# Kernel optimization log

Measured on AMD Instinct MI355X. Metric: run time of the kernel, lower is better.

## Reference

```python
import jax, jax.numpy as jnp
import numpy as np

T, B, IN_DIM, D_VALUE, D_KEY = 1024, 8, 512, 64, 64
EPS = 1e-8

def setup_inputs() -> dict:
    key = jax.random.key(0)
    ks = jax.random.split(key, 7)
    s = 1.0 / np.sqrt(IN_DIM)
    return {
        "x":  jax.random.normal(ks[0], (T, B, IN_DIM), dtype=jnp.float32),
        "Wv": jax.random.uniform(ks[1], (D_VALUE, IN_DIM), jnp.float32, -s, s),
        "bv": jax.random.uniform(ks[2], (D_VALUE,), jnp.float32, -s, s),
        "Wk": jax.random.uniform(ks[3], (D_KEY, IN_DIM), jnp.float32, -s, s),
        "bk": jax.random.uniform(ks[4], (D_KEY,), jnp.float32, -s, s),
        "Wa": jax.random.uniform(ks[5], (D_KEY, IN_DIM), jnp.float32, -s, s),
        "ba": jax.random.uniform(ks[6], (D_KEY,), jnp.float32, -s, s),
    }

def reference(x, Wv, bv, Wk, bk, Wa, ba):
    # Projections: x (T,B,in_dim) -> v (T,B,d), k (T,B,n), alpha (T,B,n)
    v = jnp.einsum('tbi,di->tbd', x, Wv) + bv
    k = jnp.einsum('tbi,ni->tbn', x, Wk) + bk
    alpha = jax.nn.sigmoid(jnp.einsum('tbi,ni->tbn', x, Wa) + ba)
    # outer product per timestep: (T,B,d,n)
    outer = jnp.einsum('tbd,tbn->tbdn', v, k)
    # log-space cumulative decay, normalized by final cumprod
    log_cumprod = jnp.cumsum(jnp.log(jnp.maximum(alpha, EPS)), axis=0)  # (T,B,n)
    cumprod = jnp.exp(log_cumprod)
    decay = cumprod / (cumprod[-1:] + EPS)
    weighted = outer * decay[:, :, None, :]  # (T,B,d,n)
    S = jnp.cumsum(weighted, axis=0)
    return S
```

## Files before the change

kernel.cpp:

```cpp
#include <hip/hip_runtime.h>
#include <math.h>

#define T_DIM  1024
#define B_DIM  8
#define IN_D   512
#define NROWS  (T_DIM * B_DIM)
#define EPSF   1e-8f
#define LOG_EPS (-18.4206807f)

#define CHUNK  16
#define NCHUNK (T_DIM / CHUNK)
#define SEG    16
#define NSEG   (T_DIM / SEG)

typedef float vfloat4 __attribute__((ext_vector_type(4)));

#define OFF_WT   0
#define OFF_V    (OFF_WT + IN_D * 192)
#define OFF_K    (OFF_V  + NROWS * 64)
#define OFF_Z    (OFF_K  + NROWS * 64)
#define OFF_SEG  (OFF_Z  + NROWS * 64)
#define OFF_TOT  (OFF_SEG + NSEG * B_DIM * 64)
#define OFF_P    (OFF_TOT + B_DIM * 64)

__global__ void k0_wt(const float* __restrict__ Wv, const float* __restrict__ Wk,
                      const float* __restrict__ Wa, float* __restrict__ Wt,
                      float* __restrict__ seg) {
    int idx = blockIdx.x * 256 + threadIdx.x;
    if (idx < NSEG * 512) seg[idx] = 0.f;
    int i = idx / 192, c = idx % 192;
    float v;
    if (c < 64)       v = Wv[c * IN_D + i];
    else if (c < 128) v = Wk[(c - 64) * IN_D + i];
    else              v = Wa[(c - 128) * IN_D + i];
    Wt[i * 192 + c] = v;
}

__global__ __launch_bounds__(256) void k1_proj(
        const float* __restrict__ x, const float* __restrict__ Wt,
        const float* __restrict__ bv, const float* __restrict__ bk, const float* __restrict__ ba,
        float* __restrict__ V, float* __restrict__ Kb, float* __restrict__ Zb,
        float* __restrict__ seg) {
    __shared__ float xs[2][32][32];
    __shared__ float wsm[2][32][192];
    const int tid  = threadIdx.x;
    const int h    = tid >> 7;
    const int t7   = tid & 127;
    const int rq   = t7 >> 4;
    const int cq   = t7 & 15;
    const int row0 = blockIdx.x * 32;

    float4 acc[4][3];
#pragma unroll
    for (int j = 0; j < 4; ++j)
#pragma unroll
        for (int m = 0; m < 3; ++m) acc[j][m] = make_float4(0.f, 0.f, 0.f, 0.f);

    for (int s = 0; s < 8; ++s) {
#pragma unroll
        for (int q = 0; q < 2; ++q) {
            int idx = tid + q * 256;
            int hh = idx >> 8, r = idx & 31, f = (idx >> 5) & 7;
            float4 v4 = reinterpret_cast<const float4*>(x)[((row0 + r) * IN_D + hh * 256 + s * 32 + f * 4) >> 2];
            xs[hh][f * 4 + 0][r] = v4.x;
            xs[hh][f * 4 + 1][r] = v4.y;
            xs[hh][f * 4 + 2][r] = v4.z;
            xs[hh][f * 4 + 3][r] = v4.w;
        }
#pragma unroll
        for (int q = 0; q < 12; ++q) {
            int idx = tid + q * 256;
            int hh = idx / 1536;
            int rem = idx - hh * 1536;
            int kk = rem / 48;
            int f  = rem - kk * 48;
            float4 v4 = reinterpret_cast<const float4*>(Wt)[((hh * 256 + s * 32 + kk) * 192 + f * 4) >> 2];
            *reinterpret_cast<float4*>(&wsm[hh][kk][f * 4]) = v4;
        }
        __syncthreads();

#pragma unroll 4
        for (int kk = 0; kk < 32; ++kk) {
            float4 xv = *reinterpret_cast<const float4*>(&xs[h][kk][rq * 4]);
#pragma unroll
            for (int m = 0; m < 3; ++m) {
                float4 wq = *reinterpret_cast<const float4*>(&wsm[h][kk][m * 64 + cq * 4]);
#pragma unroll
                for (int j = 0; j < 4; ++j) {
                    float xx = (&xv.x)[j];
                    acc[j][m].x = fmaf(xx, wq.x, acc[j][m].x);
                    acc[j][m].y = fmaf(xx, wq.y, acc[j][m].y);
                    acc[j][m].z = fmaf(xx, wq.z, acc[j][m].z);
                    acc[j][m].w = fmaf(xx, wq.w, acc[j][m].w);
                }
            }
        }
        __syncthreads();
    }

    float* red = &wsm[0][0][0];
    if (h == 1) {
#pragma unroll
        for (int j = 0; j < 4; ++j)
#pragma unroll
            for (int m = 0; m < 3; ++m)
                *reinterpret_cast<float4*>(&red[t7 * 52 + (j * 3 + m) * 4]) = acc[j][m];
    }
    __syncthreads();
    if (h == 0) {
        float4 bv4 = *reinterpret_cast<const float4*>(&bv[cq * 4]);
        float4 bk4 = *reinterpret_cast<const float4*>(&bk[cq * 4]);
        float4 ba4 = *reinterpret_cast<const float4*>(&ba[cq * 4]);
#pragma unroll
        for (int j = 0; j < 4; ++j) {
            int row = row0 + rq * 4 + j;
            float4 o0 = *reinterpret_cast<const float4*>(&red[t7 * 52 + (j * 3 + 0) * 4]);
            float4 o1 = *reinterpret_cast<const float4*>(&red[t7 * 52 + (j * 3 + 1) * 4]);
            float4 o2 = *reinterpret_cast<const float4*>(&red[t7 * 52 + (j * 3 + 2) * 4]);
            float4 r0, r1, z2, l4;
            r0.x = acc[j][0].x + o0.x + bv4.x; r0.y = acc[j][0].y + o0.y + bv4.y;
            r0.z = acc[j][0].z + o0.z + bv4.z; r0.w = acc[j][0].w + o0.w + bv4.w;
            r1.x = acc[j][1].x + o1.x + bk4.x; r1.y = acc[j][1].y + o1.y + bk4.y;
            r1.z = acc[j][1].z + o1.z + bk4.z; r1.w = acc[j][1].w + o1.w + bk4.w;
            z2.x = acc[j][2].x + o2.x + ba4.x; z2.y = acc[j][2].y + o2.y + ba4.y;
            z2.z = acc[j][2].z + o2.z + ba4.z; z2.w = acc[j][2].w + o2.w + ba4.w;
            l4.x = fmaxf(-log1pf(expf(-z2.x)), LOG_EPS);
            l4.y = fmaxf(-log1pf(expf(-z2.y)), LOG_EPS);
            l4.z = fmaxf(-log1pf(expf(-z2.z)), LOG_EPS);
            l4.w = fmaxf(-log1pf(expf(-z2.w)), LOG_EPS);
            *reinterpret_cast<float4*>(&V [row * 64 + cq * 4]) = r0;
            *reinterpret_cast<float4*>(&Kb[row * 64 + cq * 4]) = r1;
            *reinterpret_cast<float4*>(&Zb[row * 64 + cq * 4]) = l4;
            int sg = row >> 7;
            float* sp = &seg[sg * 512 + (row & 7) * 64 + cq * 4];
            atomicAdd(sp + 0, l4.x);
            atomicAdd(sp + 1, l4.y);
            atomicAdd(sp + 2, l4.z);
            atomicAdd(sp + 3, l4.w);
        }
    }
}


__global__ __launch_bounds__(256) void k3_partial(const float* __restrict__ V,
                                                  const float* __restrict__ Z,
                                                  const float* __restrict__ seg,
                                                  const float* __restrict__ Kb,
                                                  float* __restrict__ P) {
    __shared__ float vs[CHUNK * 64];
    __shared__ float wsh[CHUNK * 64];
    __shared__ float gsum[4 * 64];
    int b = blockIdx.x & 7, cch = blockIdx.x >> 3;
    int tid = threadIdx.x;
    int dg = tid >> 4, n4 = tid & 15;
    int n = tid & 63, g = tid >> 6;
    int base = b * 64 + n;

    int il = tid >> 4, f = tid & 15;
    float4 v4 = reinterpret_cast<const float4*>(V)[((cch * CHUNK + il) * 8 + b) * 16 + f];

    float run = 0.f, total = 0.f;
#pragma unroll 8
    for (int s2 = 0; s2 < NSEG; ++s2) {
        float sv = seg[s2 * 512 + base];
        if (s2 < cch) run += sv;
        total += sv;
    }
    float invden = 1.f / (expf(total) + EPSF);

    int t0 = cch * CHUNK + g * 4;
    float l0 = Z[(t0 + 0) * 512 + base];
    float l1 = Z[(t0 + 1) * 512 + base];
    float l2 = Z[(t0 + 2) * 512 + base];
    float l3 = Z[(t0 + 3) * 512 + base];
    float k0v = Kb[(t0 + 0) * 512 + base];
    float k1v = Kb[(t0 + 1) * 512 + base];
    float k2v = Kb[(t0 + 2) * 512 + base];
    float k3v = Kb[(t0 + 3) * 512 + base];
    gsum[g * 64 + n] = l0 + l1 + l2 + l3;
    reinterpret_cast<float4*>(vs)[il * 16 + f] = v4;
    __syncthreads();
    float pre = run;
#pragma unroll
    for (int g2 = 0; g2 < 3; ++g2) if (g2 < g) pre += gsum[g2 * 64 + n];
    float c0 = pre + l0, c1 = c0 + l1, c2 = c1 + l2, c3 = c2 + l3;
    wsh[(g * 4 + 0) * 64 + n] = k0v * expf(c0) * invden;
    wsh[(g * 4 + 1) * 64 + n] = k1v * expf(c1) * invden;
    wsh[(g * 4 + 2) * 64 + n] = k2v * expf(c2) * invden;
    wsh[(g * 4 + 3) * 64 + n] = k3v * expf(c3) * invden;
    __syncthreads();

    float4 acc[4];
#pragma unroll
    for (int q = 0; q < 4; ++q) acc[q] = make_float4(0.f, 0.f, 0.f, 0.f);

#pragma unroll
    for (int i = 0; i < CHUNK; ++i) {
        float4 wv = reinterpret_cast<const float4*>(wsh)[i * 16 + n4];
#pragma unroll
        for (int q = 0; q < 4; ++q) {
            float vd = vs[i * 64 + dg + 16 * q];
            acc[q].x = fmaf(vd, wv.x, acc[q].x);
            acc[q].y = fmaf(vd, wv.y, acc[q].y);
            acc[q].z = fmaf(vd, wv.z, acc[q].z);
            acc[q].w = fmaf(vd, wv.w, acc[q].w);
        }
    }
    float* Pp = P + (cch * 8 + b) * 4096;
#pragma unroll
    for (int q = 0; q < 4; ++q)
        *reinterpret_cast<float4*>(Pp + (dg + 16 * q) * 64 + 4 * n4) = acc[q];
}

__global__ __launch_bounds__(256) void k4_prefix(float* __restrict__ P) {
    int gid = blockIdx.x * 256 + threadIdx.x;
    int b = gid >> 12, dn = gid & 4095;
    float run = 0.f;
#pragma unroll
    for (int c = 0; c < NCHUNK; ++c) {
        float v = P[(c * 8 + b) * 4096 + dn];
        P[(c * 8 + b) * 4096 + dn] = run;
        run += v;
    }
}

__global__ __launch_bounds__(256) void k5_main(const float* __restrict__ V,
                                               const float* __restrict__ Z,
                                               const float* __restrict__ seg,
                                               const float* __restrict__ Kb,
                                               const float* __restrict__ P,
                                               float* __restrict__ S) {
    __shared__ float vs[CHUNK * 64];
    __shared__ float wsh[CHUNK * 64];
    __shared__ float gsum[4 * 64];
    int b = blockIdx.x & 7, cch = blockIdx.x >> 3;
    int tid = threadIdx.x;
    int dg = tid >> 4, n4 = tid & 15;
    int n = tid & 63, g = tid >> 6;
    int base = b * 64 + n;

    int il = tid >> 4, f = tid & 15;
    float4 v4 = reinterpret_cast<const float4*>(V)[((cch * CHUNK + il) * 8 + b) * 16 + f];
    vfloat4 acc[4];
    const float* Pp = P + (cch * 8 + b) * 4096;
#pragma unroll
    for (int q = 0; q < 4; ++q)
        acc[q] = *reinterpret_cast<const vfloat4*>(Pp + (dg + 16 * q) * 64 + 4 * n4);

    float run = 0.f, total = 0.f;
#pragma unroll 8
    for (int s2 = 0; s2 < NSEG; ++s2) {
        float sv = seg[s2 * 512 + base];
        if (s2 < cch) run += sv;
        total += sv;
    }
    float invden = 1.f / (expf(total) + EPSF);

    int t0 = cch * CHUNK + g * 4;
    float l0 = Z[(t0 + 0) * 512 + base];
    float l1 = Z[(t0 + 1) * 512 + base];
    float l2 = Z[(t0 + 2) * 512 + base];
    float l3 = Z[(t0 + 3) * 512 + base];
    float k0v = Kb[(t0 + 0) * 512 + base];
    float k1v = Kb[(t0 + 1) * 512 + base];
    float k2v = Kb[(t0 + 2) * 512 + base];
    float k3v = Kb[(t0 + 3) * 512 + base];
    gsum[g * 64 + n] = l0 + l1 + l2 + l3;
    reinterpret_cast<float4*>(vs)[il * 16 + f] = v4;
    __syncthreads();
    float pre = run;
#pragma unroll
    for (int g2 = 0; g2 < 3; ++g2) if (g2 < g) pre += gsum[g2 * 64 + n];
    float c0 = pre + l0, c1 = c0 + l1, c2 = c1 + l2, c3 = c2 + l3;
    wsh[(g * 4 + 0) * 64 + n] = k0v * expf(c0) * invden;
    wsh[(g * 4 + 1) * 64 + n] = k1v * expf(c1) * invden;
    wsh[(g * 4 + 2) * 64 + n] = k2v * expf(c2) * invden;
    wsh[(g * 4 + 3) * 64 + n] = k3v * expf(c3) * invden;
    __syncthreads();

#pragma unroll
    for (int i = 0; i < CHUNK; ++i) {
        float4 wv = reinterpret_cast<const float4*>(wsh)[i * 16 + n4];
        int t = cch * CHUNK + i;
        float* Sb = S + (size_t)t * 32768 + b * 4096;
#pragma unroll
        for (int q = 0; q < 4; ++q) {
            float vd = vs[i * 64 + dg + 16 * q];
            acc[q].x = fmaf(vd, wv.x, acc[q].x);
            acc[q].y = fmaf(vd, wv.y, acc[q].y);
            acc[q].z = fmaf(vd, wv.z, acc[q].z);
            acc[q].w = fmaf(vd, wv.w, acc[q].w);
            __builtin_nontemporal_store(acc[q],
                reinterpret_cast<vfloat4*>(Sb + (dg + 16 * q) * 64 + 4 * n4));
        }
    }
}

extern "C" void kernel_launch(void* const* d_in, const int* in_sizes, int n_in,
                              void* d_out, int out_size, void* d_ws, size_t ws_size,
                              hipStream_t stream) {
    const float* x  = (const float*)d_in[0];
    const float* Wv = (const float*)d_in[1];
    const float* bv = (const float*)d_in[2];
    const float* Wk = (const float*)d_in[3];
    const float* bk = (const float*)d_in[4];
    const float* Wa = (const float*)d_in[5];
    const float* ba = (const float*)d_in[6];
    float* S  = (float*)d_out;
    float* ws = (float*)d_ws;

    float* Wt  = ws + OFF_WT;
    float* V   = ws + OFF_V;
    float* Kb  = ws + OFF_K;
    float* Zb  = ws + OFF_Z;
    float* seg = ws + OFF_SEG;
    float* P   = ws + OFF_P;

    k0_wt     <<<384, 256, 0, stream>>>(Wv, Wk, Wa, Wt, seg);
    k1_proj   <<<256, 256, 0, stream>>>(x, Wt, bv, bk, ba, V, Kb, Zb, seg);
    k3_partial<<<512, 256, 0, stream>>>(V, Zb, seg, Kb, P);
    k4_prefix <<<128, 256, 0, stream>>>(P);
    k5_main   <<<512, 256, 0, stream>>>(V, Zb, seg, Kb, P, S);
}
```

Before: 216.4 us.

## Split projection K across four waves with 8-row tiles; cache decay weights for main kernel

Measured after the change: 219.6 us. About the same (+1.5%).

```diff
diff --git a/kernel.cpp b/kernel.cpp
--- a/kernel.cpp
+++ b/kernel.cpp
@@ -22,6 +22,11 @@
 #define OFF_SEG  (OFF_Z  + NROWS * 64)
 #define OFF_TOT  (OFF_SEG + NSEG * B_DIM * 64)
 #define OFF_P    (OFF_TOT + B_DIM * 64)
+#define OFF_WB   (OFF_P + NCHUNK * B_DIM * 4096)
+
+#define FMA4(A, W, C) \
+    (C).x = fmaf((A), (W).x, (C).x); (C).y = fmaf((A), (W).y, (C).y); \
+    (C).z = fmaf((A), (W).z, (C).z); (C).w = fmaf((A), (W).w, (C).w);
 
 __global__ void k0_wt(const float* __restrict__ Wv, const float* __restrict__ Wk,
                       const float* __restrict__ Wa, float* __restrict__ Wt,
@@ -41,18 +46,19 @@
         const float* __restrict__ bv, const float* __restrict__ bk, const float* __restrict__ ba,
         float* __restrict__ V, float* __restrict__ Kb, float* __restrict__ Zb,
         float* __restrict__ seg) {
-    __shared__ float xs[2][32][32];
-    __shared__ float wsm[2][32][192];
-    const int tid  = threadIdx.x;
-    const int h    = tid >> 7;
-    const int t7   = tid & 127;
-    const int rq   = t7 >> 4;
-    const int cq   = t7 & 15;
+    __shared__ float smem[14336];
+    const int tid = threadIdx.x;
+    const int h   = tid >> 6;
+    const int sl  = h >> 1;
+    const int kk0 = (h & 1) * 16;
+    const int t6  = tid & 63;
+    const int rq  = t6 >> 4;
+    const int cq  = t6 & 15;
     const int row0 = blockIdx.x * 32;
 
-    float4 acc[4][3];
-#pragma unroll
-    for (int j = 0; j < 4; ++j)
+    float4 acc[8][3];
+#pragma unroll
+    for (int j = 0; j < 8; ++j)
 #pragma unroll
         for (int m = 0; m < 3; ++m) acc[j][m] = make_float4(0.f, 0.f, 0.f, 0.f);
 
@@ -62,10 +68,10 @@
             int idx = tid + q * 256;
             int hh = idx >> 8, r = idx & 31, f = (idx >> 5) & 7;
             float4 v4 = reinterpret_cast<const float4*>(x)[((row0 + r) * IN_D + hh * 256 + s * 32 + f * 4) >> 2];
-            xs[hh][f * 4 + 0][r] = v4.x;
-            xs[hh][f * 4 + 1][r] = v4.y;
-            xs[hh][f * 4 + 2][r] = v4.z;
-            xs[hh][f * 4 + 3][r] = v4.w;
+            smem[hh * 1024 + (f * 4 + 0) * 32 + r] = v4.x;
+            smem[hh * 1024 + (f * 4 + 1) * 32 + r] = v4.y;
+            smem[hh * 1024 + (f * 4 + 2) * 32 + r] = v4.z;
+            smem[hh * 1024 + (f * 4 + 3) * 32 + r] = v4.w;
         }
 #pragma unroll
         for (int q = 0; q < 12; ++q) {
@@ -75,55 +81,86 @@
             int kk = rem / 48;
             int f  = rem - kk * 48;
             float4 v4 = reinterpret_cast<const float4*>(Wt)[((hh * 256 + s * 32 + kk) * 192 + f * 4) >> 2];
-            *reinterpret_cast<float4*>(&wsm[hh][kk][f * 4]) = v4;
+            *reinterpret_cast<float4*>(&smem[2048 + hh * 6144 + kk * 192 + f * 4]) = v4;
         }
         __syncthreads();
 
 #pragma unroll 4
-        for (int kk = 0; kk < 32; ++kk) {
-            float4 xv = *reinterpret_cast<const float4*>(&xs[h][kk][rq * 4]);
-#pragma unroll
-            for (int m = 0; m < 3; ++m) {
-                float4 wq = *reinterpret_cast<const float4*>(&wsm[h][kk][m * 64 + cq * 4]);
-#pragma unroll
-                for (int j = 0; j < 4; ++j) {
-                    float xx = (&xv.x)[j];
-                    acc[j][m].x = fmaf(xx, wq.x, acc[j][m].x);
-                    acc[j][m].y = fmaf(xx, wq.y, acc[j][m].y);
-                    acc[j][m].z = fmaf(xx, wq.z, acc[j][m].z);
-                    acc[j][m].w = fmaf(xx, wq.w, acc[j][m].w);
-                }
+        for (int k16 = 0; k16 < 16; ++k16) {
+            const int kk = kk0 + k16;
+            const float* xp = &smem[sl * 1024 + kk * 32 + rq * 8];
+            float4 xv0 = *reinterpret_cast<const float4*>(xp);
+            float4 xv1 = *reinterpret_cast<const float4*>(xp + 4);
+            const float* wp = &smem[2048 + sl * 6144 + kk * 192 + cq * 4];
+            float4 w0 = *reinterpret_cast<const float4*>(wp);
+            float4 w1 = *reinterpret_cast<const float4*>(wp + 64);
+            float4 w2 = *reinterpret_cast<const float4*>(wp + 128);
+#pragma unroll
+            for (int j = 0; j < 4; ++j) {
+                float a0 = (&xv0.x)[j];
+                float a1 = (&xv1.x)[j];
+                FMA4(a0, w0, acc[j][0]); FMA4(a0, w1, acc[j][1]); FMA4(a0, w2, acc[j][2]);
+                FMA4(a1, w0, acc[j + 4][0]); FMA4(a1, w1, acc[j + 4][1]); FMA4(a1, w2, acc[j + 4][2]);
             }
         }
         __syncthreads();
     }
 
-    float* red = &wsm[0][0][0];
-    if (h == 1) {
-#pragma unroll
-        for (int j = 0; j < 4; ++j)
+    float* red = smem;
+    if (h == 1 || h == 3) {
+        float* rg = red + (h >> 1) * 6144;
+#pragma unroll
+        for (int jr = 0; jr < 8; ++jr)
 #pragma unroll
             for (int m = 0; m < 3; ++m)
-                *reinterpret_cast<float4*>(&red[t7 * 52 + (j * 3 + m) * 4]) = acc[j][m];
+#pragma unroll
+                for (int c = 0; c < 4; ++c)
+                    rg[((jr * 3 + m) * 4 + c) * 64 + t6] = (&acc[jr][m].x)[c];
+    }
+    __syncthreads();
+    if (h == 0 || h == 2) {
+        float* rg = red + (h >> 1) * 6144;
+#pragma unroll
+        for (int jr = 0; jr < 8; ++jr)
+#pragma unroll
+            for (int m = 0; m < 3; ++m)
+#pragma unroll
+                for (int c = 0; c < 4; ++c)
+                    (&acc[jr][m].x)[c] += rg[((jr * 3 + m) * 4 + c) * 64 + t6];
+    }
+    __syncthreads();
+    if (h == 2) {
+#pragma unroll
+        for (int jr = 0; jr < 8; ++jr)
+#pragma unroll
+            for (int m = 0; m < 3; ++m)
+#pragma unroll
+                for (int c = 0; c < 4; ++c)
+                    red[((jr * 3 + m) * 4 + c) * 64 + t6] = (&acc[jr][m].x)[c];
     }
     __syncthreads();
     if (h == 0) {
+#pragma unroll
+        for (int jr = 0; jr < 8; ++jr)
+#pragma unroll
+            for (int m = 0; m < 3; ++m)
+#pragma unroll
+                for (int c = 0; c < 4; ++c)
+                    (&acc[jr][m].x)[c] += red[((jr * 3 + m) * 4 + c) * 64 + t6];
+
         float4 bv4 = *reinterpret_cast<const float4*>(&bv[cq * 4]);
         float4 bk4 = *reinterpret_cast<const float4*>(&bk[cq * 4]);
         float4 ba4 = *reinterpret_cast<const float4*>(&ba[cq * 4]);
 #pragma unroll
-        for (int j = 0; j < 4; ++j) {
-            int row = row0 + rq * 4 + j;
-            float4 o0 = *reinterpret_cast<const float4*>(&red[t7 * 52 + (j * 3 + 0) * 4]);
-            float4 o1 = *reinterpret_cast<const float4*>(&red[t7 * 52 + (j * 3 + 1) * 4]);
-            float4 o2 = *reinterpret_cast<const float4*>(&red[t7 * 52 + (j * 3 + 2) * 4]);
+        for (int jr = 0; jr < 8; ++jr) {
+            int row = row0 + rq * 8 + jr;
             float4 r0, r1, z2, l4;
-            r0.x = acc[j][0].x + o0.x + bv4.x; r0.y = acc[j][0].y + o0.y + bv4.y;
-            r0.z = acc[j][0].z + o0.z + bv4.z; r0.w = acc[j][0].w + o0.w + bv4.w;
-            r1.x = acc[j][1].x + o1.x + bk4.x; r1.y = acc[j][1].y + o1.y + bk4.y;
-            r1.z = acc[j][1].z + o1.z + bk4.z; r1.w = acc[j][1].w + o1.w + bk4.w;
-            z2.x = acc[j][2].x + o2.x + ba4.x; z2.y = acc[j][2].y + o2.y + ba4.y;
-            z2.z = acc[j][2].z + o2.z + ba4.z; z2.w = acc[j][2].w + o2.w + ba4.w;
+            r0.x = acc[jr][0].x + bv4.x; r0.y = acc[jr][0].y + bv4.y;
+            r0.z = acc[jr][0].z + bv4.z; r0.w = acc[jr][0].w + bv4.w;
+            r1.x = acc[jr][1].x + bk4.x; r1.y = acc[jr][1].y + bk4.y;
+            r1.z = acc[jr][1].z + bk4.z; r1.w = acc[jr][1].w + bk4.w;
+            z2.x = acc[jr][2].x + ba4.x; z2.y = acc[jr][2].y + ba4.y;
+            z2.z = acc[jr][2].z + ba4.z; z2.w = acc[jr][2].w + ba4.w;
             l4.x = fmaxf(-log1pf(expf(-z2.x)), LOG_EPS);
             l4.y = fmaxf(-log1pf(expf(-z2.y)), LOG_EPS);
             l4.z = fmaxf(-log1pf(expf(-z2.z)), LOG_EPS);
@@ -131,8 +168,7 @@
             *reinterpret_cast<float4*>(&V [row * 64 + cq * 4]) = r0;
             *reinterpret_cast<float4*>(&Kb[row * 64 + cq * 4]) = r1;
             *reinterpret_cast<float4*>(&Zb[row * 64 + cq * 4]) = l4;
-            int sg = row >> 7;
-            float* sp = &seg[sg * 512 + (row & 7) * 64 + cq * 4];
+            float* sp = &seg[(row >> 7) * 512 + (row & 7) * 64 + cq * 4];
             atomicAdd(sp + 0, l4.x);
             atomicAdd(sp + 1, l4.y);
             atomicAdd(sp + 2, l4.z);
@@ -141,12 +177,12 @@
     }
 }
 
-
 __global__ __launch_bounds__(256) void k3_partial(const float* __restrict__ V,
                                                   const float* __restrict__ Z,
                                                   const float* __restrict__ seg,
                                                   const float* __restrict__ Kb,
-                                                  float* __restrict__ P) {
+                                                  float* __restrict__ P,
+                                                  float* __restrict__ Wb) {
     __shared__ float vs[CHUNK * 64];
     __shared__ float wsh[CHUNK * 64];
     __shared__ float gsum[4 * 64];
@@ -155,8 +191,8 @@
     int dg = tid >> 4, n4 = tid & 15;
     int n = tid & 63, g = tid >> 6;
     int base = b * 64 + n;
-
     int il = tid >> 4, f = tid & 15;
+
     float4 v4 = reinterpret_cast<const float4*>(V)[((cch * CHUNK + il) * 8 + b) * 16 + f];
 
     float run = 0.f, total = 0.f;
@@ -190,6 +226,9 @@
     wsh[(g * 4 + 3) * 64 + n] = k3v * expf(c3) * invden;
     __syncthreads();
 
+    reinterpret_cast<float4*>(Wb)[(cch * 8 + b) * 256 + il * 16 + f] =
+        reinterpret_cast<const float4*>(wsh)[il * 16 + f];
+
     float4 acc[4];
 #pragma unroll
     for (int q = 0; q < 4; ++q) acc[q] = make_float4(0.f, 0.f, 0.f, 0.f);
@@ -225,57 +264,25 @@
 }
 
 __global__ __launch_bounds__(256) void k5_main(const float* __restrict__ V,
-                                               const float* __restrict__ Z,
-                                               const float* __restrict__ seg,
-                                               const float* __restrict__ Kb,
+                                               const float* __restrict__ Wb,
                                                const float* __restrict__ P,
                                                float* __restrict__ S) {
     __shared__ float vs[CHUNK * 64];
     __shared__ float wsh[CHUNK * 64];
-    __shared__ float gsum[4 * 64];
     int b = blockIdx.x & 7, cch = blockIdx.x >> 3;
     int tid = threadIdx.x;
     int dg = tid >> 4, n4 = tid & 15;
-    int n = tid & 63, g = tid >> 6;
-    int base = b * 64 + n;
-
     int il = tid >> 4, f = tid & 15;
+
     float4 v4 = reinterpret_cast<const float4*>(V)[((cch * CHUNK + il) * 8 + b) * 16 + f];
+    float4 w4 = reinterpret_cast<const float4*>(Wb)[(cch * 8 + b) * 256 + il * 16 + f];
     vfloat4 acc[4];
     const float* Pp = P + (cch * 8 + b) * 4096;
 #pragma unroll
     for (int q = 0; q < 4; ++q)
         acc[q] = *reinterpret_cast<const vfloat4*>(Pp + (dg + 16 * q) * 64 + 4 * n4);
-
-    float run = 0.f, total = 0.f;
-#pragma unroll 8
-    for (int s2 = 0; s2 < NSEG; ++s2) {
-        float sv = seg[s2 * 512 + base];
-        if (s2 < cch) run += sv;
-        total += sv;
-    }
-    float invden = 1.f / (expf(total) + EPSF);
-
-    int t0 = cch * CHUNK + g * 4;
-    float l0 = Z[(t0 + 0) * 512 + base];
-    float l1 = Z[(t0 + 1) * 512 + base];
-    float l2 = Z[(t0 + 2) * 512 + base];
-    float l3 = Z[(t0 + 3) * 512 + base];
-    float k0v = Kb[(t0 + 0) * 512 + base];
-    float k1v = Kb[(t0 + 1) * 512 + base];
-    float k2v = Kb[(t0 + 2) * 512 + base];
-    float k3v = Kb[(t0 + 3) * 512 + base];
-    gsum[g * 64 + n] = l0 + l1 + l2 + l3;
-    reinterpret_cast<float4*>(vs)[il * 16 + f] = v4;
-    __syncthreads();
-    float pre = run;
-#pragma unroll
-    for (int g2 = 0; g2 < 3; ++g2) if (g2 < g) pre += gsum[g2 * 64 + n];
-    float c0 = pre + l0, c1 = c0 + l1, c2 = c1 + l2, c3 = c2 + l3;
-    wsh[(g * 4 + 0) * 64 + n] = k0v * expf(c0) * invden;
-    wsh[(g * 4 + 1) * 64 + n] = k1v * expf(c1) * invden;
-    wsh[(g * 4 + 2) * 64 + n] = k2v * expf(c2) * invden;
-    wsh[(g * 4 + 3) * 64 + n] = k3v * expf(c3) * invden;
+    reinterpret_cast<float4*>(vs)[il * 16 + f]  = v4;
+    reinterpret_cast<float4*>(wsh)[il * 16 + f] = w4;
     __syncthreads();
 
 #pragma unroll
@@ -315,10 +322,11 @@
     float* Zb  = ws + OFF_Z;
     float* seg = ws + OFF_SEG;
     float* P   = ws + OFF_P;
+    float* Wb  = ws + OFF_WB;
 
     k0_wt     <<<384, 256, 0, stream>>>(Wv, Wk, Wa, Wt, seg);
     k1_proj   <<<256, 256, 0, stream>>>(x, Wt, bv, bk, ba, V, Kb, Zb, seg);
-    k3_partial<<<512, 256, 0, stream>>>(V, Zb, seg, Kb, P);
+    k3_partial<<<512, 256, 0, stream>>>(V, Zb, seg, Kb, P, Wb);
     k4_prefix <<<128, 256, 0, stream>>>(P);
-    k5_main   <<<512, 256, 0, stream>>>(V, Zb, seg, Kb, P, S);
-}
+    k5_main   <<<512, 256, 0, stream>>>(V, Wb, P, S);
+}
```
